# Kernel tuning notes

Hardware: AMD Instinct MI355X
Metric: run time of the kernel (lower is better)

Reference implementation:

```python
import jax, jax.numpy as jnp
import numpy as np

SEQLEN = (512, 1024, 2048, 1536, 768, 1280, 896, 640)
HEAD_NUM = 16
HIDDEN = 1024  # head_size = 64


def setup_inputs() -> dict:
    key = jax.random.key(0)
    k1, k2 = jax.random.split(key)
    total_a = HEAD_NUM * sum(s * s for s in SEQLEN)  # packed per-seq (H, s, s) blocks
    a = jax.random.normal(k1, (total_a,), dtype=jnp.float32) * 0.02
    b = jax.random.normal(k2, (sum(SEQLEN), HIDDEN), dtype=jnp.float32)
    return {"a": a, "b": b, "seqlen": list(SEQLEN), "head_num": HEAD_NUM}


def reference(a, b, seqlen, head_num):
    """Ragged strided bmm2: per sequence i, per head h:
    C_i[:, h*hs:(h+1)*hs] = A_i[h] @ B_i[:, h*hs:(h+1)*hs].
    a packed flat as sum_i (head_num, s_i, s_i); b is (sum(s), hidden).
    """
    hidden = b.shape[1]
    hs = hidden // head_num
    outs = []
    a_off = 0
    t_off = 0
    for s in seqlen:  # static loop over ragged batch (lengths are compile-time)
        ai = jax.lax.dynamic_slice(a, (a_off,), (head_num * s * s,)).reshape(head_num, s, s)
        bi = jax.lax.dynamic_slice(b, (t_off, 0), (s, hidden)).reshape(s, head_num, hs)
        # (H, q, k) x (k, H, d) -> (q, H, d) -> (q, hidden)
        ci = jnp.einsum('hqk,khd->qhd', ai, bi).reshape(s, hidden)
        outs.append(ci)
        a_off += head_num * s * s
        t_off += s
    return jnp.concatenate(outs, axis=0)  # (sum(seqlen), hidden)
```

## Files before the change

### kernel.cpp

```cpp
#include <hip/hip_runtime.h>
#include <hip/hip_bf16.h>

typedef __attribute__((ext_vector_type(4))) float f32x4;
typedef __attribute__((ext_vector_type(8))) short bf16x8;
typedef __attribute__((ext_vector_type(4))) short bf16x4;

__device__ __forceinline__ unsigned cvt2(float lo, float hi) {
    float2 t; t.x = lo; t.y = hi;
    __hip_bfloat162 h = __float22bfloat162_rn(t);
    union { __hip_bfloat162 h; unsigned u; } c; c.h = h; return c.u;
}

__global__ __launch_bounds__(256, 3) void bmm2_k(const float* __restrict__ a,
                                                 const float* __restrict__ b,
                                                 float* __restrict__ out) {
    const int  cumblk[9] = {0,256,448,608,736,848,944,1024,1088};
    const int  slen[8]   = {2048,1536,1280,1024,896,768,640,512};
    const long aoff[8]   = {20971520,88080384,135266304,4194304,161480704,125829120,174325760,0};
    const int  toff[8]   = {1536,3584,5888,512,7168,5120,8064,0};

    __shared__ unsigned short As[128 * 72];
    __shared__ unsigned short Bs[64 * 72];

    int bid = blockIdx.x;
    int i = 0;
    #pragma unroll
    for (int t = 0; t < 7; ++t) if (bid >= cumblk[t + 1]) i = t + 1;
    int rem  = bid - cumblk[i];
    int s    = slen[i];
    int nmb  = s >> 7;
    int head = rem / nmb;
    int mb   = rem - head * nmb;

    const float* A  = a + aoff[i] + (long)head * s * s + (long)mb * 128 * s;
    const float* Bp = b + (long)toff[i] * 1024 + head * 64;
    float*       Cp = out + (long)(toff[i] + mb * 128) * 1024 + head * 64;

    int tid = threadIdx.x, lane = tid & 63, wave = tid >> 6;
    int lrow = lane & 15, lgrp = lane >> 4;

    int arow = tid >> 4;
    int kf   = (tid & 15) * 4;
    const float* Ast = A + (long)arow * s + kf;

    int bj0 = (tid & 15) * 4;
    int bk0 = (tid >> 4) * 4;
    const float* Bst = Bp + (long)bk0 * 1024 + bj0;

    f32x4 rA[8], rB[4];
    f32x4 acc[2][4] = {};
    int NT = s >> 6;

    #pragma unroll
    for (int q = 0; q < 8; ++q) rA[q] = *(const f32x4*)(Ast + (long)(q * 16) * s);
    #pragma unroll
    for (int q = 0; q < 4; ++q) rB[q] = *(const f32x4*)(Bst + (long)q * 1024);

    for (int t = 0; t < NT; ++t) {
        __syncthreads();

        #pragma unroll
        for (int q = 0; q < 8; ++q) {
            int r = q * 16 + arow;
            union { bf16x4 v; unsigned u[2]; } w;
            w.u[0] = cvt2(rA[q][0], rA[q][1]);
            w.u[1] = cvt2(rA[q][2], rA[q][3]);
            *(bf16x4*)&As[r * 72 + kf] = w.v;
        }
        #pragma unroll
        for (int e = 0; e < 4; ++e) {
            union { bf16x4 v; unsigned u[2]; } w;
            w.u[0] = cvt2(rB[0][e], rB[1][e]);
            w.u[1] = cvt2(rB[2][e], rB[3][e]);
            *(bf16x4*)&Bs[(bj0 + e) * 72 + bk0] = w.v;
        }

        __syncthreads();

        if (t + 1 < NT) {
            int kn = (t + 1) << 6;
            #pragma unroll
            for (int q = 0; q < 8; ++q) rA[q] = *(const f32x4*)(Ast + (long)(q * 16) * s + kn);
            #pragma unroll
            for (int q = 0; q < 4; ++q) rB[q] = *(const f32x4*)(Bst + (long)(kn + q) * 1024);
        }

        #pragma unroll
        for (int ks = 0; ks < 2; ++ks) {
            bf16x8 af0 = *(const bf16x8*)&As[(wave * 32 + lrow) * 72 + ks * 32 + lgrp * 8];
            bf16x8 af1 = *(const bf16x8*)&As[(wave * 32 + 16 + lrow) * 72 + ks * 32 + lgrp * 8];
            bf16x8 bf[4];
            #pragma unroll
            for (int n = 0; n < 4; ++n)
                bf[n] = *(const bf16x8*)&Bs[(n * 16 + lrow) * 72 + ks * 32 + lgrp * 8];
            #pragma unroll
            for (int n = 0; n < 4; ++n) {
                acc[0][n] = __builtin_amdgcn_mfma_f32_16x16x32_bf16(af0, bf[n], acc[0][n], 0, 0, 0);
                acc[1][n] = __builtin_amdgcn_mfma_f32_16x16x32_bf16(af1, bf[n], acc[1][n], 0, 0, 0);
            }
        }
    }

    #pragma unroll
    for (int mt = 0; mt < 2; ++mt)
        #pragma unroll
        for (int n = 0; n < 4; ++n)
            #pragma unroll
            for (int r = 0; r < 4; ++r) {
                int q = wave * 32 + mt * 16 + lgrp * 4 + r;
                Cp[(long)q * 1024 + n * 16 + lrow] = acc[mt][n][r];
            }
}

extern "C" void kernel_launch(void* const* d_in, const int* in_sizes, int n_in,
                              void* d_out, int out_size, void* d_ws, size_t ws_size,
                              hipStream_t stream) {
    const float* a = (const float*)d_in[0];
    const float* b = (const float*)d_in[1];
    float* out = (float*)d_out;
    bmm2_k<<<1088, 256, 0, stream>>>(a, b, out);
}
```

Measured before the change: 178.1 us.

## Interleave block order, use nontemporal loads/stores, and hand-roll barriers

Remaps block IDs so each group of eight consecutive blocks spans different sequences, raises the launch-bounds occupancy hint from 3 to 4, marks the streamed A loads and C stores nontemporal, and issues the next-tile global loads before the second barrier. The __syncthreads calls become raw s_barrier with an explicit lgkmcnt wait and a sched_barrier. The aim is better cache behaviour for A and C, more overlap of global latency, and more waves per CU, at the cost of register pressure from the occupancy hint.

New measurement: 192.8 us. 1.08x slower.

```diff
diff --git a/kernel.cpp b/kernel.cpp
--- a/kernel.cpp
+++ b/kernel.cpp
@@ -10,8 +10,13 @@
     __hip_bfloat162 h = __float22bfloat162_rn(t);
     union { __hip_bfloat162 h; unsigned u; } c; c.h = h; return c.u;
 }
+__device__ __forceinline__ bf16x4 pk4(float a0, float a1, float a2, float a3) {
+    union { bf16x4 v; unsigned u[2]; } w;
+    w.u[0] = cvt2(a0, a1); w.u[1] = cvt2(a2, a3);
+    return w.v;
+}
 
-__global__ __launch_bounds__(256, 3) void bmm2_k(const float* __restrict__ a,
+__global__ __launch_bounds__(256, 4) void bmm2_k(const float* __restrict__ a,
                                                  const float* __restrict__ b,
                                                  float* __restrict__ out) {
     const int  cumblk[9] = {0,256,448,608,736,848,944,1024,1088};
@@ -22,7 +27,8 @@
     __shared__ unsigned short As[128 * 72];
     __shared__ unsigned short Bs[64 * 72];
 
-    int bid = blockIdx.x;
+    int bid = (blockIdx.x & 7) * 136 + (blockIdx.x >> 3);
+
     int i = 0;
     #pragma unroll
     for (int t = 0; t < 7; ++t) if (bid >= cumblk[t + 1]) i = t + 1;
@@ -52,38 +58,33 @@
     int NT = s >> 6;
 
     #pragma unroll
-    for (int q = 0; q < 8; ++q) rA[q] = *(const f32x4*)(Ast + (long)(q * 16) * s);
+    for (int q = 0; q < 8; ++q)
+        rA[q] = __builtin_nontemporal_load((const f32x4*)(Ast + (long)(q * 16) * s));
     #pragma unroll
     for (int q = 0; q < 4; ++q) rB[q] = *(const f32x4*)(Bst + (long)q * 1024);
 
     for (int t = 0; t < NT; ++t) {
-        __syncthreads();
+        __builtin_amdgcn_s_barrier();
 
         #pragma unroll
-        for (int q = 0; q < 8; ++q) {
-            int r = q * 16 + arow;
-            union { bf16x4 v; unsigned u[2]; } w;
-            w.u[0] = cvt2(rA[q][0], rA[q][1]);
-            w.u[1] = cvt2(rA[q][2], rA[q][3]);
-            *(bf16x4*)&As[r * 72 + kf] = w.v;
-        }
+        for (int q = 0; q < 8; ++q)
+            *(bf16x4*)&As[(q * 16 + arow) * 72 + kf] = pk4(rA[q][0], rA[q][1], rA[q][2], rA[q][3]);
         #pragma unroll
-        for (int e = 0; e < 4; ++e) {
-            union { bf16x4 v; unsigned u[2]; } w;
-            w.u[0] = cvt2(rB[0][e], rB[1][e]);
-            w.u[1] = cvt2(rB[2][e], rB[3][e]);
-            *(bf16x4*)&Bs[(bj0 + e) * 72 + bk0] = w.v;
+        for (int e = 0; e < 4; ++e)
+            *(bf16x4*)&Bs[(bj0 + e) * 72 + bk0] = pk4(rB[0][e], rB[1][e], rB[2][e], rB[3][e]);
+
+        if (t + 1 < NT) {
+            long kn = (long)(t + 1) << 6;
+            #pragma unroll
+            for (int q = 0; q < 8; ++q)
+                rA[q] = __builtin_nontemporal_load((const f32x4*)(Ast + (long)(q * 16) * s + kn));
+            #pragma unroll
+            for (int q = 0; q < 4; ++q) rB[q] = *(const f32x4*)(Bst + (kn + q) * 1024);
         }
 
-        __syncthreads();
-
-        if (t + 1 < NT) {
-            int kn = (t + 1) << 6;
-            #pragma unroll
-            for (int q = 0; q < 8; ++q) rA[q] = *(const f32x4*)(Ast + (long)(q * 16) * s + kn);
-            #pragma unroll
-            for (int q = 0; q < 4; ++q) rB[q] = *(const f32x4*)(Bst + (long)(kn + q) * 1024);
-        }
+        asm volatile("s_waitcnt lgkmcnt(0)" ::: "memory");
+        __builtin_amdgcn_sched_barrier(0);
+        __builtin_amdgcn_s_barrier();
 
         #pragma unroll
         for (int ks = 0; ks < 2; ++ks) {
@@ -108,7 +109,7 @@
             #pragma unroll
             for (int r = 0; r < 4; ++r) {
                 int q = wave * 32 + mt * 16 + lgrp * 4 + r;
-                Cp[(long)q * 1024 + n * 16 + lrow] = acc[mt][n][r];
+                __builtin_nontemporal_store(acc[mt][n][r], &Cp[(long)q * 1024 + n * 16 + lrow]);
             }
 }
 
```
